# Kernel tuning notes

Measured on AMD Instinct MI355X. Metric: run time of the kernel, lower is better.

The kernel has to match this reference:

```python
import jax, jax.numpy as jnp
import numpy as np

DIM = 512
NUM_EXPERTS = 8
HID = 4 * DIM
B, S = 2, 2048


def setup_inputs() -> dict:
    key = jax.random.key(0)
    ks = jax.random.split(key, 7)
    sc = 0.02
    x = jax.random.normal(ks[0], (B, S, DIM), dtype=jnp.float32)
    Wr = jax.random.normal(ks[1], (DIM, NUM_EXPERTS), dtype=jnp.float32) * sc
    br = jnp.zeros((NUM_EXPERTS,), dtype=jnp.float32)
    W1 = jax.random.normal(ks[2], (NUM_EXPERTS, DIM, HID), dtype=jnp.float32) * sc
    b1 = jnp.zeros((NUM_EXPERTS, HID), dtype=jnp.float32)
    W2 = jax.random.normal(ks[3], (NUM_EXPERTS, HID, DIM), dtype=jnp.float32) * sc
    b2 = jnp.zeros((NUM_EXPERTS, DIM), dtype=jnp.float32)
    return {"x": x, "Wr": Wr, "br": br, "W1": W1, "b1": b1, "W2": W2, "b2": b2}


def reference(x, Wr, br, W1, b1, W2, b2):
    b, s, d = x.shape
    E = Wr.shape[1]
    xf = x.reshape(-1, d)                                   # [N, d]
    N = xf.shape[0]
    logits = xf @ Wr + br                                   # [N, E]
    probs = jax.nn.softmax(logits, axis=-1)
    top_w, top_idx = jax.lax.top_k(probs, 2)                # [N, 2]
    top_w = jax.nn.softmax(top_w, axis=-1)                  # renormalize top-2
    # combine weight per (token, expert); topk indices are distinct so add is safe
    comb = jnp.zeros((N, E), dtype=xf.dtype)
    comb = comb.at[jnp.arange(N)[:, None], top_idx].add(top_w)  # [N, E]
    # dense per-expert MLP (eval mode: dropout is identity); exact GELU as nn.GELU
    h = jax.nn.gelu(jnp.einsum('nd,edf->enf', xf, W1) + b1[:, None, :], approximate=False)
    y = jnp.einsum('enf,efd->end', h, W2) + b2[:, None, :]  # [E, N, d]
    out = jnp.einsum('end,ne->nd', y, comb)                 # weighted combine
    # load-balancing loss
    load = jnp.zeros((E,), dtype=jnp.float32).at[top_idx.reshape(-1)].add(1.0)
    load = load / load.sum()
    lb_loss = jnp.sum((load - 1.0 / E) ** 2)
    return out.reshape(b, s, d), lb_loss, load
```

## Files before the change

kernel.cpp:

```cpp
#include <hip/hip_runtime.h>
#include <hip/hip_bf16.h>

#define DIMD 512
#define NEXP 8
#define HIDN 2048
#define NTOK 4096
#define NASG 8192

typedef short bf16x8 __attribute__((ext_vector_type(8)));
typedef float f32x4 __attribute__((ext_vector_type(4)));

__device__ inline unsigned short f2bf(float f) {
  __hip_bfloat16 h = __float2bfloat16(f);
  return __builtin_bit_cast(unsigned short, h);
}

__device__ inline void gl16(const void* g, void* l) {
  __builtin_amdgcn_global_load_lds(
      (const __attribute__((address_space(1))) unsigned int*)g,
      (__attribute__((address_space(3))) unsigned int*)l, 16, 0, 0);
}

#define PIPE_WAIT4_BAR() do { \
  asm volatile("s_waitcnt vmcnt(4)" ::: "memory"); \
  __builtin_amdgcn_s_barrier(); \
  __builtin_amdgcn_sched_barrier(0); } while (0)
#define PIPE_WAIT0_BAR() do { \
  asm volatile("s_waitcnt vmcnt(0)" ::: "memory"); \
  __builtin_amdgcn_s_barrier(); \
  __builtin_amdgcn_sched_barrier(0); } while (0)
#define PIPE_POST_BAR() do { \
  asm volatile("" ::: "memory"); \
  __builtin_amdgcn_sched_barrier(0); \
  __builtin_amdgcn_s_barrier(); } while (0)

__global__ __launch_bounds__(256) void transpose_both_kernel(
    const float* __restrict__ W1, const float* __restrict__ W2,
    unsigned short* __restrict__ w1t, unsigned short* __restrict__ w2t) {
  __shared__ float tile[64][65];
  int z = blockIdx.z;
  int e = z & 7;
  const float* src; unsigned short* dst; int R, C, r0, c0;
  if (z < 8) { src = W1; dst = w1t; R = DIMD; C = HIDN; c0 = blockIdx.x * 64; r0 = blockIdx.y * 64; }
  else       { src = W2; dst = w2t; R = HIDN; C = DIMD; r0 = blockIdx.x * 64; c0 = blockIdx.y * 64; }
  const float* s = src + (size_t)e * R * C;
  unsigned short* d = dst + (size_t)e * R * C;
  for (int i = threadIdx.x; i < 4096; i += 256) {
    int r = i >> 6, c = i & 63;
    tile[r][c] = s[(size_t)(r0 + r) * C + (c0 + c)];
  }
  __syncthreads();
  for (int i = threadIdx.x; i < 2048; i += 256) {
    int c = i >> 5;
    int r = (i & 31) * 2;
    unsigned lo = f2bf(tile[r][c]);
    unsigned hi = f2bf(tile[r + 1][c]);
    *reinterpret_cast<unsigned*>(d + (size_t)(c0 + c) * R + (r0 + r)) = lo | (hi << 16);
  }
}

__global__ __launch_bounds__(256) void router_kernel(const float* __restrict__ x,
                                                     const float* __restrict__ Wr,
                                                     const float* __restrict__ br,
                                                     int* __restrict__ tidx,
                                                     float* __restrict__ tw,
                                                     unsigned short* __restrict__ xb) {
  int lane = threadIdx.x & 63;
  int n = blockIdx.x * 4 + (threadIdx.x >> 6);
  const float* xr = x + (size_t)n * DIMD;
  unsigned short* xbr = xb + (size_t)n * DIMD;
  float acc[NEXP];
#pragma unroll
  for (int e = 0; e < NEXP; ++e) acc[e] = 0.f;
#pragma unroll
  for (int it = 0; it < 2; ++it) {
    int d0 = it * 256 + lane * 4;
    float4 xv = *reinterpret_cast<const float4*>(xr + d0);
    unsigned p0 = (unsigned)f2bf(xv.x) | ((unsigned)f2bf(xv.y) << 16);
    unsigned p1 = (unsigned)f2bf(xv.z) | ((unsigned)f2bf(xv.w) << 16);
    *reinterpret_cast<uint2*>(xbr + d0) = make_uint2(p0, p1);
    const float* wr = Wr + (size_t)d0 * NEXP;
#pragma unroll
    for (int j = 0; j < 4; ++j) {
      float xj = (&xv.x)[j];
#pragma unroll
      for (int e = 0; e < NEXP; ++e) acc[e] += xj * wr[j * NEXP + e];
    }
  }
#pragma unroll
  for (int e = 0; e < NEXP; ++e) {
    float v = acc[e];
#pragma unroll
    for (int off = 32; off > 0; off >>= 1) v += __shfl_xor(v, off, 64);
    acc[e] = v + br[e];
  }
  if (lane == 0) {
    float m = acc[0];
    for (int e = 1; e < NEXP; ++e) m = fmaxf(m, acc[e]);
    float p[NEXP], s = 0.f;
    for (int e = 0; e < NEXP; ++e) { p[e] = expf(acc[e] - m); s += p[e]; }
    float inv = 1.f / s;
    for (int e = 0; e < NEXP; ++e) p[e] *= inv;
    int i0 = 0; float p0 = p[0];
    for (int e = 1; e < NEXP; ++e) if (p[e] > p0) { p0 = p[e]; i0 = e; }
    int i1 = (i0 == 0) ? 1 : 0; float p1 = p[i1];
    for (int e = 0; e < NEXP; ++e) if (e != i0 && p[e] > p1) { p1 = p[e]; i1 = e; }
    float t = expf(p1 - p0);
    float w0 = 1.f / (1.f + t);
    tidx[2 * n] = i0; tidx[2 * n + 1] = i1;
    tw[2 * n] = w0; tw[2 * n + 1] = t * w0;
  }
}

__global__ __launch_bounds__(1024) void route_pack_kernel(const int* __restrict__ tidx,
                                                          int* __restrict__ off,
                                                          int* __restrict__ list,
                                                          float* __restrict__ out_tail) {
  int tid = threadIdx.x;
  int wv = tid >> 6, lane = tid & 63;

  int ids[8];
#pragma unroll
  for (int j = 0; j < 8; ++j) ids[j] = tidx[tid * 8 + j];

  int c[NEXP];
#pragma unroll
  for (int e = 0; e < NEXP; ++e) c[e] = 0;
#pragma unroll
  for (int j = 0; j < 8; ++j)
#pragma unroll
    for (int e = 0; e < NEXP; ++e) c[e] += (ids[j] == e) ? 1 : 0;

  int inc[NEXP];
#pragma unroll
  for (int e = 0; e < NEXP; ++e) {
    int v = c[e];
#pragma unroll
    for (int d = 1; d < 64; d <<= 1) {
      int t = __shfl_up(v, d, 64);
      if (lane >= d) v += t;
    }
    inc[e] = v;
  }

  __shared__ int wtot[NEXP][16];
  __shared__ int wbase[NEXP][16];
  __shared__ int ebase[NEXP];
  if (lane == 63) {
#pragma unroll
    for (int e = 0; e < NEXP; ++e) wtot[e][wv] = inc[e];
  }
  __syncthreads();
  if (tid == 0) {
    int o = 0;
    float lb = 0.f;
    for (int e = 0; e < NEXP; ++e) {
      int s = 0;
      for (int w = 0; w < 16; ++w) { wbase[e][w] = s; s += wtot[e][w]; }
      ebase[e] = o;
      off[e] = o;
      o += s;
      float l = (float)s / (float)NASG;
      out_tail[1 + e] = l;
      float dd = l - 0.125f;
      lb += dd * dd;
    }
    off[NEXP] = o;
    out_tail[0] = lb;
  }
  __syncthreads();

  int pos[NEXP];
#pragma unroll
  for (int e = 0; e < NEXP; ++e)
    pos[e] = ebase[e] + wbase[e][wv] + (inc[e] - c[e]);

#pragma unroll
  for (int j = 0; j < 8; ++j) {
    int e = ids[j];
    int p = 0;
#pragma unroll
    for (int k = 0; k < NEXP; ++k)
      if (e == k) { p = pos[k]; pos[k] = p + 1; }
    list[p] = tid * 8 + j;
  }
}


__global__ __launch_bounds__(256) void gemm1_kernel(
    const unsigned short* __restrict__ xb,
    const unsigned short* __restrict__ w1t,
    const float* __restrict__ b1,
    const int* __restrict__ off,
    const int* __restrict__ list,
    unsigned short* __restrict__ H) {
  int e = blockIdx.x;
  int offe = off[e];
  int cnt_e = off[e + 1] - offe;
  int n0 = blockIdx.y * 128;
  int m0 = blockIdx.z * 128;
  if (m0 >= cnt_e) return;

  __shared__ char ldsb[36864];

  int tid = threadIdx.x, wv = tid >> 6, lane = tid & 63;
  int rp = lane >> 3, sl = lane & 7;
  int sx = sl ^ rp;
  int rowadd = rp * 2 + (sx >> 2);
  int kq = sx & 3;

  const unsigned short* w1e = w1t + (size_t)e * HIDN * DIMD;
  const unsigned short* asrc[2];
  const unsigned short* bsrc[2];
#pragma unroll
  for (int i = 0; i < 2; ++i) {
    int r = wv * 32 + i * 16 + rowadd;
    int rr = m0 + r;
    int tok = 0;
    if (rr < cnt_e) tok = list[offe + rr] >> 1;
    asrc[i] = xb + (size_t)tok * DIMD + kq * 8;
    bsrc[i] = w1e + (size_t)(n0 + r) * DIMD + kq * 8;
  }
  int dstA0 = wv * 2048;
  int dstA1 = wv * 2048 + 1024;

  f32x4 zero = {0.f, 0.f, 0.f, 0.f};
  f32x4 acc[4][4];
#pragma unroll
  for (int m = 0; m < 4; ++m)
#pragma unroll
    for (int n = 0; n < 4; ++n) acc[m][n] = zero;

  int wave_m = wv >> 1, wave_n = wv & 1;
  int lane16 = lane & 15, kq4 = lane >> 4;
  int ra[4], rb[4];
#pragma unroll
  for (int m = 0; m < 4; ++m) {
    int r = wave_m * 64 + m * 16 + lane16;
    ra[m] = (r >> 1) * 128 + ((((kq4 + (r & 1) * 4)) ^ ((r >> 1) & 7)) << 4);
    int rn = wave_n * 64 + m * 16 + lane16;
    rb[m] = (rn >> 1) * 128 + ((((kq4 + (rn & 1) * 4)) ^ ((rn >> 1) & 7)) << 4);
  }

  auto stage = [&](char* nb, int k0) {
    gl16(asrc[0] + k0, nb + dstA0);
    gl16(asrc[1] + k0, nb + dstA1);
    gl16(bsrc[0] + k0, nb + 8192 + dstA0);
    gl16(bsrc[1] + k0, nb + 8192 + dstA1);
  };
  auto compute = [&](const char* cb) {
    bf16x8 af[4], bfr[4];
#pragma unroll
    for (int m = 0; m < 4; ++m) af[m] = *reinterpret_cast<const bf16x8*>(cb + ra[m]);
#pragma unroll
    for (int n = 0; n < 4; ++n) bfr[n] = *reinterpret_cast<const bf16x8*>(cb + 8192 + rb[n]);
#pragma unroll
    for (int m = 0; m < 4; ++m)
#pragma unroll
      for (int n = 0; n < 4; ++n)
        acc[m][n] = __builtin_amdgcn_mfma_f32_16x16x32_bf16(af[m], bfr[n], acc[m][n], 0, 0, 0);
  };

  const int T = DIMD / 32;
  stage(ldsb, 0);
  stage(ldsb + 16384, 32);
  for (int t = 0; t < T - 2; ++t) {
    char* cb = ldsb + (t & 1) * 16384;
    PIPE_WAIT4_BAR();
    compute(cb);
    PIPE_POST_BAR();
    stage(cb, (t + 2) * 32);
  }
  PIPE_WAIT4_BAR();
  compute(ldsb + ((T - 2) & 1) * 16384);
  PIPE_POST_BAR();
  PIPE_WAIT0_BAR();
  compute(ldsb + ((T - 1) & 1) * 16384);
  PIPE_POST_BAR();

  unsigned short* Ct = (unsigned short*)ldsb;
  const float* b1e = b1 + e * HIDN;
#pragma unroll
  for (int n = 0; n < 4; ++n) {
    int cl = wave_n * 64 + n * 16 + lane16;
    float bias = b1e[n0 + cl];
#pragma unroll
    for (int m = 0; m < 4; ++m) {
#pragma unroll
      for (int q = 0; q < 4; ++q) {
        int rl = wave_m * 64 + m * 16 + kq4 * 4 + q;
        float v = acc[m][n][q] + bias;
        float g = 0.5f * v * (1.f + erff(v * 0.70710678118654752f));
        Ct[rl * 136 + cl] = f2bf(g);
      }
    }
  }
  __syncthreads();
  for (int u = tid; u < 2048; u += 256) {
    int rl = u >> 4, c8 = (u & 15) * 8;
    int r = m0 + rl;
    if (r < cnt_e) {
      uint4 v = *reinterpret_cast<const uint4*>(Ct + rl * 136 + c8);
      *reinterpret_cast<uint4*>(H + (size_t)(offe + r) * HIDN + n0 + c8) = v;
    }
  }
}

__global__ __launch_bounds__(256) void gemm2_kernel(
    const unsigned short* __restrict__ H,
    const unsigned short* __restrict__ w2t,
    const float* __restrict__ b2,
    const int* __restrict__ off,
    const int* __restrict__ list,
    const float* __restrict__ tw,
    float* __restrict__ Yw) {
  int e = blockIdx.x;
  int offe = off[e];
  int cnt_e = off[e + 1] - offe;
  int n0 = blockIdx.y * 128;
  int m0 = blockIdx.z * 128;
  if (m0 >= cnt_e) return;

  __shared__ char ldsb[32768];

  int tid = threadIdx.x, wv = tid >> 6, lane = tid & 63;
  int rp = lane >> 3, sl = lane & 7;
  int sx = sl ^ rp;
  int rowadd = rp * 2 + (sx >> 2);
  int kq = sx & 3;

  const unsigned short* w2e = w2t + (size_t)e * DIMD * HIDN;
  const unsigned short* asrc[2];
  const unsigned short* bsrc[2];
#pragma unroll
  for (int i = 0; i < 2; ++i) {
    int r = wv * 32 + i * 16 + rowadd;
    int rowa = offe + m0 + r;
    if (rowa > NASG - 1) rowa = NASG - 1;
    asrc[i] = H + (size_t)rowa * HIDN + kq * 8;
    bsrc[i] = w2e + (size_t)(n0 + r) * HIDN + kq * 8;
  }
  int dstA0 = wv * 2048;
  int dstA1 = wv * 2048 + 1024;

  f32x4 zero = {0.f, 0.f, 0.f, 0.f};
  f32x4 acc[4][4];
#pragma unroll
  for (int m = 0; m < 4; ++m)
#pragma unroll
    for (int n = 0; n < 4; ++n) acc[m][n] = zero;

  int wave_m = wv >> 1, wave_n = wv & 1;
  int lane16 = lane & 15, kq4 = lane >> 4;
  int ra[4], rb[4];
#pragma unroll
  for (int m = 0; m < 4; ++m) {
    int r = wave_m * 64 + m * 16 + lane16;
    ra[m] = (r >> 1) * 128 + ((((kq4 + (r & 1) * 4)) ^ ((r >> 1) & 7)) << 4);
    int rn = wave_n * 64 + m * 16 + lane16;
    rb[m] = (rn >> 1) * 128 + ((((kq4 + (rn & 1) * 4)) ^ ((rn >> 1) & 7)) << 4);
  }

  auto stage = [&](char* nb, int k0) {
    gl16(asrc[0] + k0, nb + dstA0);
    gl16(asrc[1] + k0, nb + dstA1);
    gl16(bsrc[0] + k0, nb + 8192 + dstA0);
    gl16(bsrc[1] + k0, nb + 8192 + dstA1);
  };
  auto compute = [&](const char* cb) {
    bf16x8 af[4], bfr[4];
#pragma unroll
    for (int m = 0; m < 4; ++m) af[m] = *reinterpret_cast<const bf16x8*>(cb + ra[m]);
#pragma unroll
    for (int n = 0; n < 4; ++n) bfr[n] = *reinterpret_cast<const bf16x8*>(cb + 8192 + rb[n]);
#pragma unroll
    for (int m = 0; m < 4; ++m)
#pragma unroll
      for (int n = 0; n < 4; ++n)
        acc[m][n] = __builtin_amdgcn_mfma_f32_16x16x32_bf16(af[m], bfr[n], acc[m][n], 0, 0, 0);
  };

  const int T = HIDN / 32;
  stage(ldsb, 0);
  stage(ldsb + 16384, 32);
  for (int t = 0; t < T - 2; ++t) {
    char* cb = ldsb + (t & 1) * 16384;
    PIPE_WAIT4_BAR();
    compute(cb);
    PIPE_POST_BAR();
    stage(cb, (t + 2) * 32);
  }
  PIPE_WAIT4_BAR();
  compute(ldsb + ((T - 2) & 1) * 16384);
  PIPE_POST_BAR();
  PIPE_WAIT0_BAR();
  compute(ldsb + ((T - 1) & 1) * 16384);
  PIPE_POST_BAR();

  const float* b2e = b2 + e * DIMD;
  float bias[4];
#pragma unroll
  for (int n = 0; n < 4; ++n) bias[n] = b2e[n0 + wave_n * 64 + n * 16 + lane16];
#pragma unroll
  for (int m = 0; m < 4; ++m) {
#pragma unroll
    for (int q = 0; q < 4; ++q) {
      int r = m0 + wave_m * 64 + m * 16 + kq4 * 4 + q;
      if (r < cnt_e) {
        int a = list[offe + r];
        float w = tw[a];
        float* yrow = Yw + (size_t)a * DIMD;
#pragma unroll
        for (int n = 0; n < 4; ++n) {
          int col = n0 + wave_n * 64 + n * 16 + lane16;
          yrow[col] = w * (acc[m][n][q] + bias[n]);
        }
      }
    }
  }
}

__global__ __launch_bounds__(256) void combine_kernel(const float* __restrict__ Yw,
                                                      float* __restrict__ out) {
  int i = (blockIdx.x * 256 + threadIdx.x) * 4;
  int n = i >> 9;
  int d = i & 511;
  float4 a = *reinterpret_cast<const float4*>(Yw + (size_t)(2 * n) * DIMD + d);
  float4 b = *reinterpret_cast<const float4*>(Yw + (size_t)(2 * n + 1) * DIMD + d);
  float4 o;
  o.x = a.x + b.x; o.y = a.y + b.y; o.z = a.z + b.z; o.w = a.w + b.w;
  *reinterpret_cast<float4*>(out + i) = o;
}

extern "C" void kernel_launch(void* const* d_in, const int* in_sizes, int n_in,
                              void* d_out, int out_size, void* d_ws, size_t ws_size,
                              hipStream_t stream) {
  const float* x  = (const float*)d_in[0];
  const float* Wr = (const float*)d_in[1];
  const float* br = (const float*)d_in[2];
  const float* W1 = (const float*)d_in[3];
  const float* b1 = (const float*)d_in[4];
  const float* W2 = (const float*)d_in[5];
  const float* b2 = (const float*)d_in[6];
  float* out = (float*)d_out;

  char* ws = (char*)d_ws;
  unsigned short* xb  = (unsigned short*)ws;  ws += (size_t)NTOK * DIMD * 2;
  unsigned short* w1t = (unsigned short*)ws;  ws += (size_t)NEXP * HIDN * DIMD * 2;
  unsigned short* w2t = (unsigned short*)ws;  ws += (size_t)NEXP * DIMD * HIDN * 2;
  unsigned short* H   = (unsigned short*)ws;  ws += (size_t)NASG * HIDN * 2;
  float* Yw = (float*)ws;                     ws += (size_t)NASG * DIMD * 4;
  float* tw = (float*)ws;                     ws += (size_t)NASG * 4;
  int* tidx = (int*)ws;                       ws += (size_t)NASG * 4;
  int* list = (int*)ws;                       ws += (size_t)NASG * 4;
  int* offp = (int*)ws;

  transpose_both_kernel<<<dim3(32, 8, 16), 256, 0, stream>>>(W1, W2, w1t, w2t);
  router_kernel<<<NTOK / 4, 256, 0, stream>>>(x, Wr, br, tidx, tw, xb);
  route_pack_kernel<<<1, 1024, 0, stream>>>(tidx, offp, list, out + (size_t)NTOK * DIMD);
  gemm1_kernel<<<dim3(NEXP, HIDN / 128, NASG / 128), 256, 0, stream>>>(xb, w1t, b1, offp, list, H);
  gemm2_kernel<<<dim3(NEXP, DIMD / 128, NASG / 128), 256, 0, stream>>>(H, w2t, b2, offp, list, tw, Yw);
  combine_kernel<<<2048, 256, 0, stream>>>(Yw, out);
}
```

Before: 118.3 us.

## Use 256-row M tiles, triple-buffered pipeline, split-K gemm2 with combine epilogue

```diff
diff --git a/kernel.cpp b/kernel.cpp
--- a/kernel.cpp
+++ b/kernel.cpp
@@ -21,8 +21,12 @@
       (__attribute__((address_space(3))) unsigned int*)l, 16, 0, 0);
 }
 
-#define PIPE_WAIT4_BAR() do { \
-  asm volatile("s_waitcnt vmcnt(4)" ::: "memory"); \
+#define PIPE_WAIT12_BAR() do { \
+  asm volatile("s_waitcnt vmcnt(12)" ::: "memory"); \
+  __builtin_amdgcn_s_barrier(); \
+  __builtin_amdgcn_sched_barrier(0); } while (0)
+#define PIPE_WAIT6_BAR() do { \
+  asm volatile("s_waitcnt vmcnt(6)" ::: "memory"); \
   __builtin_amdgcn_s_barrier(); \
   __builtin_amdgcn_sched_barrier(0); } while (0)
 #define PIPE_WAIT0_BAR() do { \
@@ -187,7 +191,7 @@
 }
 
 
-__global__ __launch_bounds__(256) void gemm1_kernel(
+__global__ __launch_bounds__(256, 2) void gemm1_kernel(
     const unsigned short* __restrict__ xb,
     const unsigned short* __restrict__ w1t,
     const float* __restrict__ b1,
@@ -198,10 +202,10 @@
   int offe = off[e];
   int cnt_e = off[e + 1] - offe;
   int n0 = blockIdx.y * 128;
-  int m0 = blockIdx.z * 128;
+  int m0 = blockIdx.z * 256;
   if (m0 >= cnt_e) return;
 
-  __shared__ char ldsb[36864];
+  __shared__ char ldsb[73728];
 
   int tid = threadIdx.x, wv = tid >> 6, lane = tid & 63;
   int rp = lane >> 3, sl = lane & 7;
@@ -210,52 +214,61 @@
   int kq = sx & 3;
 
   const unsigned short* w1e = w1t + (size_t)e * HIDN * DIMD;
-  const unsigned short* asrc[2];
+  const unsigned short* asrc[4];
   const unsigned short* bsrc[2];
 #pragma unroll
-  for (int i = 0; i < 2; ++i) {
-    int r = wv * 32 + i * 16 + rowadd;
+  for (int i = 0; i < 4; ++i) {
+    int r = wv * 64 + i * 16 + rowadd;
     int rr = m0 + r;
     int tok = 0;
     if (rr < cnt_e) tok = list[offe + rr] >> 1;
     asrc[i] = xb + (size_t)tok * DIMD + kq * 8;
+  }
+#pragma unroll
+  for (int i = 0; i < 2; ++i) {
+    int r = wv * 32 + i * 16 + rowadd;
     bsrc[i] = w1e + (size_t)(n0 + r) * DIMD + kq * 8;
   }
-  int dstA0 = wv * 2048;
-  int dstA1 = wv * 2048 + 1024;
+  int dA = wv * 4096;
+  int dB = 16384 + wv * 2048;
 
   f32x4 zero = {0.f, 0.f, 0.f, 0.f};
-  f32x4 acc[4][4];
-#pragma unroll
-  for (int m = 0; m < 4; ++m)
+  f32x4 acc[8][4];
+#pragma unroll
+  for (int m = 0; m < 8; ++m)
 #pragma unroll
     for (int n = 0; n < 4; ++n) acc[m][n] = zero;
 
   int wave_m = wv >> 1, wave_n = wv & 1;
   int lane16 = lane & 15, kq4 = lane >> 4;
-  int ra[4], rb[4];
-#pragma unroll
-  for (int m = 0; m < 4; ++m) {
-    int r = wave_m * 64 + m * 16 + lane16;
+  int ra[8], rb[4];
+#pragma unroll
+  for (int m = 0; m < 8; ++m) {
+    int r = wave_m * 128 + m * 16 + lane16;
     ra[m] = (r >> 1) * 128 + ((((kq4 + (r & 1) * 4)) ^ ((r >> 1) & 7)) << 4);
-    int rn = wave_n * 64 + m * 16 + lane16;
-    rb[m] = (rn >> 1) * 128 + ((((kq4 + (rn & 1) * 4)) ^ ((rn >> 1) & 7)) << 4);
+  }
+#pragma unroll
+  for (int n = 0; n < 4; ++n) {
+    int rn = wave_n * 64 + n * 16 + lane16;
+    rb[n] = (rn >> 1) * 128 + ((((kq4 + (rn & 1) * 4)) ^ ((rn >> 1) & 7)) << 4);
   }
 
   auto stage = [&](char* nb, int k0) {
-    gl16(asrc[0] + k0, nb + dstA0);
-    gl16(asrc[1] + k0, nb + dstA1);
-    gl16(bsrc[0] + k0, nb + 8192 + dstA0);
-    gl16(bsrc[1] + k0, nb + 8192 + dstA1);
+    gl16(asrc[0] + k0, nb + dA);
+    gl16(asrc[1] + k0, nb + dA + 1024);
+    gl16(asrc[2] + k0, nb + dA + 2048);
+    gl16(asrc[3] + k0, nb + dA + 3072);
+    gl16(bsrc[0] + k0, nb + dB);
+    gl16(bsrc[1] + k0, nb + dB + 1024);
   };
   auto compute = [&](const char* cb) {
-    bf16x8 af[4], bfr[4];
-#pragma unroll
-    for (int m = 0; m < 4; ++m) af[m] = *reinterpret_cast<const bf16x8*>(cb + ra[m]);
-#pragma unroll
-    for (int n = 0; n < 4; ++n) bfr[n] = *reinterpret_cast<const bf16x8*>(cb + 8192 + rb[n]);
-#pragma unroll
-    for (int m = 0; m < 4; ++m)
+    bf16x8 af[8], bfr[4];
+#pragma unroll
+    for (int m = 0; m < 8; ++m) af[m] = *reinterpret_cast<const bf16x8*>(cb + ra[m]);
+#pragma unroll
+    for (int n = 0; n < 4; ++n) bfr[n] = *reinterpret_cast<const bf16x8*>(cb + 16384 + rb[n]);
+#pragma unroll
+    for (int m = 0; m < 8; ++m)
 #pragma unroll
       for (int n = 0; n < 4; ++n)
         acc[m][n] = __builtin_amdgcn_mfma_f32_16x16x32_bf16(af[m], bfr[n], acc[m][n], 0, 0, 0);
@@ -263,65 +276,69 @@
 
   const int T = DIMD / 32;
   stage(ldsb, 0);
-  stage(ldsb + 16384, 32);
-  for (int t = 0; t < T - 2; ++t) {
-    char* cb = ldsb + (t & 1) * 16384;
-    PIPE_WAIT4_BAR();
+  stage(ldsb + 24576, 32);
+  stage(ldsb + 49152, 64);
+  int cyc = 0;
+  for (int t = 0; t < T; ++t) {
+    char* cb = ldsb + cyc * 24576;
+    if (t <= T - 3) PIPE_WAIT12_BAR();
+    else if (t == T - 2) PIPE_WAIT6_BAR();
+    else PIPE_WAIT0_BAR();
     compute(cb);
     PIPE_POST_BAR();
-    stage(cb, (t + 2) * 32);
-  }
-  PIPE_WAIT4_BAR();
-  compute(ldsb + ((T - 2) & 1) * 16384);
-  PIPE_POST_BAR();
-  PIPE_WAIT0_BAR();
-  compute(ldsb + ((T - 1) & 1) * 16384);
-  PIPE_POST_BAR();
+    if (t <= T - 4) stage(cb, (t + 3) * 32);
+    cyc = (cyc == 2) ? 0 : cyc + 1;
+  }
 
   unsigned short* Ct = (unsigned short*)ldsb;
   const float* b1e = b1 + e * HIDN;
-#pragma unroll
-  for (int n = 0; n < 4; ++n) {
-    int cl = wave_n * 64 + n * 16 + lane16;
-    float bias = b1e[n0 + cl];
-#pragma unroll
-    for (int m = 0; m < 4; ++m) {
-#pragma unroll
-      for (int q = 0; q < 4; ++q) {
-        int rl = wave_m * 64 + m * 16 + kq4 * 4 + q;
-        float v = acc[m][n][q] + bias;
-        float g = 0.5f * v * (1.f + erff(v * 0.70710678118654752f));
-        Ct[rl * 136 + cl] = f2bf(g);
+  for (int c = 0; c < 2; ++c) {
+    if (wave_m == c) {
+#pragma unroll
+      for (int n = 0; n < 4; ++n) {
+        int cl = wave_n * 64 + n * 16 + lane16;
+        float bias = b1e[n0 + cl];
+#pragma unroll
+        for (int m = 0; m < 8; ++m) {
+#pragma unroll
+          for (int q = 0; q < 4; ++q) {
+            int rl = m * 16 + kq4 * 4 + q;
+            float v = acc[m][n][q] + bias;
+            float g = 0.5f * v * (1.f + erff(v * 0.70710678118654752f));
+            Ct[rl * 136 + cl] = f2bf(g);
+          }
+        }
       }
     }
-  }
-  __syncthreads();
-  for (int u = tid; u < 2048; u += 256) {
-    int rl = u >> 4, c8 = (u & 15) * 8;
-    int r = m0 + rl;
-    if (r < cnt_e) {
-      uint4 v = *reinterpret_cast<const uint4*>(Ct + rl * 136 + c8);
-      *reinterpret_cast<uint4*>(H + (size_t)(offe + r) * HIDN + n0 + c8) = v;
-    }
-  }
-}
-
-__global__ __launch_bounds__(256) void gemm2_kernel(
+    __syncthreads();
+    for (int u = tid; u < 2048; u += 256) {
+      int rl = u >> 4, c8 = (u & 15) * 8;
+      int r = m0 + c * 128 + rl;
+      if (r < cnt_e) {
+        uint4 v = *reinterpret_cast<const uint4*>(Ct + rl * 136 + c8);
+        *reinterpret_cast<uint4*>(H + (size_t)(offe + r) * HIDN + n0 + c8) = v;
+      }
+    }
+    __syncthreads();
+  }
+}
+
+__global__ __launch_bounds__(256, 2) void gemm2_kernel(
     const unsigned short* __restrict__ H,
     const unsigned short* __restrict__ w2t,
-    const float* __restrict__ b2,
     const int* __restrict__ off,
     const int* __restrict__ list,
-    const float* __restrict__ tw,
     float* __restrict__ Yw) {
   int e = blockIdx.x;
   int offe = off[e];
   int cnt_e = off[e + 1] - offe;
-  int n0 = blockIdx.y * 128;
-  int m0 = blockIdx.z * 128;
+  int n0 = (blockIdx.y >> 1) * 128;
+  int khalf = blockIdx.y & 1;
+  int kbase = khalf * (HIDN / 2);
+  int m0 = blockIdx.z * 256;
   if (m0 >= cnt_e) return;
 
-  __shared__ char ldsb[32768];
+  __shared__ char ldsb[73728];
 
   int tid = threadIdx.x, wv = tid >> 6, lane = tid & 63;
   int rp = lane >> 3, sl = lane & 7;
@@ -330,90 +347,94 @@
   int kq = sx & 3;
 
   const unsigned short* w2e = w2t + (size_t)e * DIMD * HIDN;
-  const unsigned short* asrc[2];
+  const unsigned short* asrc[4];
   const unsigned short* bsrc[2];
+#pragma unroll
+  for (int i = 0; i < 4; ++i) {
+    int r = wv * 64 + i * 16 + rowadd;
+    int rowa = offe + m0 + r;
+    if (rowa > NASG - 1) rowa = NASG - 1;
+    asrc[i] = H + (size_t)rowa * HIDN + kbase + kq * 8;
+  }
 #pragma unroll
   for (int i = 0; i < 2; ++i) {
     int r = wv * 32 + i * 16 + rowadd;
-    int rowa = offe + m0 + r;
-    if (rowa > NASG - 1) rowa = NASG - 1;
-    asrc[i] = H + (size_t)rowa * HIDN + kq * 8;
-    bsrc[i] = w2e + (size_t)(n0 + r) * HIDN + kq * 8;
-  }
-  int dstA0 = wv * 2048;
-  int dstA1 = wv * 2048 + 1024;
+    bsrc[i] = w2e + (size_t)(n0 + r) * HIDN + kbase + kq * 8;
+  }
+  int dA = wv * 4096;
+  int dB = 16384 + wv * 2048;
 
   f32x4 zero = {0.f, 0.f, 0.f, 0.f};
-  f32x4 acc[4][4];
-#pragma unroll
-  for (int m = 0; m < 4; ++m)
+  f32x4 acc[8][4];
+#pragma unroll
+  for (int m = 0; m < 8; ++m)
 #pragma unroll
     for (int n = 0; n < 4; ++n) acc[m][n] = zero;
 
   int wave_m = wv >> 1, wave_n = wv & 1;
   int lane16 = lane & 15, kq4 = lane >> 4;
-  int ra[4], rb[4];
-#pragma unroll
-  for (int m = 0; m < 4; ++m) {
-    int r = wave_m * 64 + m * 16 + lane16;
+  int ra[8], rb[4];
+#pragma unroll
+  for (int m = 0; m < 8; ++m) {
+    int r = wave_m * 128 + m * 16 + lane16;
     ra[m] = (r >> 1) * 128 + ((((kq4 + (r & 1) * 4)) ^ ((r >> 1) & 7)) << 4);
-    int rn = wave_n * 64 + m * 16 + lane16;
-    rb[m] = (rn >> 1) * 128 + ((((kq4 + (rn & 1) * 4)) ^ ((rn >> 1) & 7)) << 4);
+  }
+#pragma unroll
+  for (int n = 0; n < 4; ++n) {
+    int rn = wave_n * 64 + n * 16 + lane16;
+    rb[n] = (rn >> 1) * 128 + ((((kq4 + (rn & 1) * 4)) ^ ((rn >> 1) & 7)) << 4);
   }
 
   auto stage = [&](char* nb, int k0) {
-    gl16(asrc[0] + k0, nb + dstA0);
-    gl16(asrc[1] + k0, nb + dstA1);
-    gl16(bsrc[0] + k0, nb + 8192 + dstA0);
-    gl16(bsrc[1] + k0, nb + 8192 + dstA1);
+    gl16(asrc[0] + k0, nb + dA);
+    gl16(asrc[1] + k0, nb + dA + 1024);
+    gl16(asrc[2] + k0, nb + dA + 2048);
+    gl16(asrc[3] + k0, nb + dA + 3072);
+    gl16(bsrc[0] + k0, nb + dB);
+    gl16(bsrc[1] + k0, nb + dB + 1024);
   };
   auto compute = [&](const char* cb) {
-    bf16x8 af[4], bfr[4];
-#pragma unroll
-    for (int m = 0; m < 4; ++m) af[m] = *reinterpret_cast<const bf16x8*>(cb + ra[m]);
-#pragma unroll
-    for (int n = 0; n < 4; ++n) bfr[n] = *reinterpret_cast<const bf16x8*>(cb + 8192 + rb[n]);
-#pragma unroll
-    for (int m = 0; m < 4; ++m)
+    bf16x8 af[8], bfr[4];
+#pragma unroll
+    for (int m = 0; m < 8; ++m) af[m] = *reinterpret_cast<const bf16x8*>(cb + ra[m]);
+#pragma unroll
+    for (int n = 0; n < 4; ++n) bfr[n] = *reinterpret_cast<const bf16x8*>(cb + 16384 + rb[n]);
+#pragma unroll
+    for (int m = 0; m < 8; ++m)
 #pragma unroll
       for (int n = 0; n < 4; ++n)
         acc[m][n] = __builtin_amdgcn_mfma_f32_16x16x32_bf16(af[m], bfr[n], acc[m][n], 0, 0, 0);
   };
 
-  const int T = HIDN / 32;
+  const int T = (HIDN / 2) / 32;
   stage(ldsb, 0);
-  stage(ldsb + 16384, 32);
-  for (int t = 0; t < T - 2; ++t) {
-    char* cb = ldsb + (t & 1) * 16384;
-    PIPE_WAIT4_BAR();
+  stage(ldsb + 24576, 32);
+  stage(ldsb + 49152, 64);
+  int cyc = 0;
+  for (int t = 0; t < T; ++t) {
+    char* cb = ldsb + cyc * 24576;
+    if (t <= T - 3) PIPE_WAIT12_BAR();
+    else if (t == T - 2) PIPE_WAIT6_BAR();
+    else PIPE_WAIT0_BAR();
     compute(cb);
     PIPE_POST_BAR();
-    stage(cb, (t + 2) * 32);
-  }
-  PIPE_WAIT4_BAR();
-  compute(ldsb + ((T - 2) & 1) * 16384);
-  PIPE_POST_BAR();
-  PIPE_WAIT0_BAR();
-  compute(ldsb + ((T - 1) & 1) * 16384);
-  PIPE_POST_BAR();
-
-  const float* b2e = b2 + e * DIMD;
-  float bias[4];
-#pragma unroll
-  for (int n = 0; n < 4; ++n) bias[n] = b2e[n0 + wave_n * 64 + n * 16 + lane16];
-#pragma unroll
-  for (int m = 0; m < 4; ++m) {
+    if (t <= T - 4) stage(cb, (t + 3) * 32);
+    cyc = (cyc == 2) ? 0 : cyc + 1;
+  }
+
+  float* Ywp = Yw + (size_t)khalf * NASG * DIMD;
+#pragma unroll
+  for (int m = 0; m < 8; ++m) {
 #pragma unroll
     for (int q = 0; q < 4; ++q) {
-      int r = m0 + wave_m * 64 + m * 16 + kq4 * 4 + q;
+      int r = m0 + wave_m * 128 + m * 16 + kq4 * 4 + q;
       if (r < cnt_e) {
         int a = list[offe + r];
-        float w = tw[a];
-        float* yrow = Yw + (size_t)a * DIMD;
+        float* yrow = Ywp + (size_t)a * DIMD;
 #pragma unroll
         for (int n = 0; n < 4; ++n) {
           int col = n0 + wave_n * 64 + n * 16 + lane16;
-          yrow[col] = w * (acc[m][n][q] + bias[n]);
+          yrow[col] = acc[m][n][q];
         }
       }
     }
@@ -421,14 +442,28 @@
 }
 
 __global__ __launch_bounds__(256) void combine_kernel(const float* __restrict__ Yw,
+                                                      const int* __restrict__ tidx,
+                                                      const float* __restrict__ tw,
+                                                      const float* __restrict__ b2,
                                                       float* __restrict__ out) {
+  const float* Y1 = Yw + (size_t)NASG * DIMD;
   int i = (blockIdx.x * 256 + threadIdx.x) * 4;
   int n = i >> 9;
   int d = i & 511;
-  float4 a = *reinterpret_cast<const float4*>(Yw + (size_t)(2 * n) * DIMD + d);
-  float4 b = *reinterpret_cast<const float4*>(Yw + (size_t)(2 * n + 1) * DIMD + d);
+  int a0 = 2 * n, a1 = 2 * n + 1;
+  float w0 = tw[a0], w1 = tw[a1];
+  int e0 = tidx[a0], e1 = tidx[a1];
+  float4 p0 = *reinterpret_cast<const float4*>(Yw + (size_t)a0 * DIMD + d);
+  float4 q0 = *reinterpret_cast<const float4*>(Y1 + (size_t)a0 * DIMD + d);
+  float4 p1 = *reinterpret_cast<const float4*>(Yw + (size_t)a1 * DIMD + d);
+  float4 q1 = *reinterpret_cast<const float4*>(Y1 + (size_t)a1 * DIMD + d);
+  float4 c0 = *reinterpret_cast<const float4*>(b2 + (size_t)e0 * DIMD + d);
+  float4 c1 = *reinterpret_cast<const float4*>(b2 + (size_t)e1 * DIMD + d);
   float4 o;
-  o.x = a.x + b.x; o.y = a.y + b.y; o.z = a.z + b.z; o.w = a.w + b.w;
+  o.x = w0 * (p0.x + q0.x + c0.x) + w1 * (p1.x + q1.x + c1.x);
+  o.y = w0 * (p0.y + q0.y + c0.y) + w1 * (p1.y + q1.y + c1.y);
+  o.z = w0 * (p0.z + q0.z + c0.z) + w1 * (p1.z + q1.z + c1.z);
+  o.w = w0 * (p0.w + q0.w + c0.w) + w1 * (p1.w + q1.w + c1.w);
   *reinterpret_cast<float4*>(out + i) = o;
 }
 
@@ -449,7 +484,7 @@
   unsigned short* w1t = (unsigned short*)ws;  ws += (size_t)NEXP * HIDN * DIMD * 2;
   unsigned short* w2t = (unsigned short*)ws;  ws += (size_t)NEXP * DIMD * HIDN * 2;
   unsigned short* H   = (unsigned short*)ws;  ws += (size_t)NASG * HIDN * 2;
-  float* Yw = (float*)ws;                     ws += (size_t)NASG * DIMD * 4;
+  float* Yw = (float*)ws;                     ws += (size_t)2 * NASG * DIMD * 4;
   float* tw = (float*)ws;                     ws += (size_t)NASG * 4;
   int* tidx = (int*)ws;                       ws += (size_t)NASG * 4;
   int* list = (int*)ws;                       ws += (size_t)NASG * 4;
@@ -458,7 +493,7 @@
   transpose_both_kernel<<<dim3(32, 8, 16), 256, 0, stream>>>(W1, W2, w1t, w2t);
   router_kernel<<<NTOK / 4, 256, 0, stream>>>(x, Wr, br, tidx, tw, xb);
   route_pack_kernel<<<1, 1024, 0, stream>>>(tidx, offp, list, out + (size_t)NTOK * DIMD);
-  gemm1_kernel<<<dim3(NEXP, HIDN / 128, NASG / 128), 256, 0, stream>>>(xb, w1t, b1, offp, list, H);
-  gemm2_kernel<<<dim3(NEXP, DIMD / 128, NASG / 128), 256, 0, stream>>>(H, w2t, b2, offp, list, tw, Yw);
-  combine_kernel<<<2048, 256, 0, stream>>>(Yw, out);
-}
+  gemm1_kernel<<<dim3(NEXP, HIDN / 128, NASG / 256), 256, 0, stream>>>(xb, w1t, b1, offp, list, H);
+  gemm2_kernel<<<dim3(NEXP, (DIMD / 128) * 2, NASG / 256), 256, 0, stream>>>(H, w2t, offp, list, Yw);
+  combine_kernel<<<2048, 256, 0, stream>>>(Yw, tidx, tw, b2, out);
+}
```

Result: slower. 145.5 us (+23.0%).

## Split gemm2 along K into two halves with 64-wide N tiles, reduce in combine

Applied to the files above, without the earlier changes.

```diff
diff --git a/kernel.cpp b/kernel.cpp
--- a/kernel.cpp
+++ b/kernel.cpp
@@ -23,6 +23,10 @@
 
 #define PIPE_WAIT4_BAR() do { \
   asm volatile("s_waitcnt vmcnt(4)" ::: "memory"); \
+  __builtin_amdgcn_s_barrier(); \
+  __builtin_amdgcn_sched_barrier(0); } while (0)
+#define PIPE_WAIT3_BAR() do { \
+  asm volatile("s_waitcnt vmcnt(3)" ::: "memory"); \
   __builtin_amdgcn_s_barrier(); \
   __builtin_amdgcn_sched_barrier(0); } while (0)
 #define PIPE_WAIT0_BAR() do { \
@@ -309,19 +313,20 @@
 __global__ __launch_bounds__(256) void gemm2_kernel(
     const unsigned short* __restrict__ H,
     const unsigned short* __restrict__ w2t,
-    const float* __restrict__ b2,
     const int* __restrict__ off,
     const int* __restrict__ list,
-    const float* __restrict__ tw,
     float* __restrict__ Yw) {
   int e = blockIdx.x;
   int offe = off[e];
   int cnt_e = off[e + 1] - offe;
-  int n0 = blockIdx.y * 128;
+  int y = blockIdx.y;
+  int khalf = y >> 3;
+  int n0 = (y & 7) * 64;
+  int kbase = khalf * (HIDN / 2);
   int m0 = blockIdx.z * 128;
   if (m0 >= cnt_e) return;
 
-  __shared__ char ldsb[32768];
+  __shared__ char ldsb[24576];
 
   int tid = threadIdx.x, wv = tid >> 6, lane = tid & 63;
   int rp = lane >> 3, sl = lane & 7;
@@ -331,76 +336,74 @@
 
   const unsigned short* w2e = w2t + (size_t)e * DIMD * HIDN;
   const unsigned short* asrc[2];
-  const unsigned short* bsrc[2];
+  const unsigned short* bsrc0;
 #pragma unroll
   for (int i = 0; i < 2; ++i) {
     int r = wv * 32 + i * 16 + rowadd;
     int rowa = offe + m0 + r;
     if (rowa > NASG - 1) rowa = NASG - 1;
-    asrc[i] = H + (size_t)rowa * HIDN + kq * 8;
-    bsrc[i] = w2e + (size_t)(n0 + r) * HIDN + kq * 8;
-  }
-  int dstA0 = wv * 2048;
-  int dstA1 = wv * 2048 + 1024;
+    asrc[i] = H + (size_t)rowa * HIDN + kbase + kq * 8;
+  }
+  {
+    int r = wv * 16 + rowadd;
+    bsrc0 = w2e + (size_t)(n0 + r) * HIDN + kbase + kq * 8;
+  }
+  int dA0 = wv * 2048;
+  int dA1 = wv * 2048 + 1024;
+  int dB = 8192 + wv * 1024;
 
   f32x4 zero = {0.f, 0.f, 0.f, 0.f};
-  f32x4 acc[4][4];
+  f32x4 acc[4][2];
 #pragma unroll
   for (int m = 0; m < 4; ++m)
 #pragma unroll
-    for (int n = 0; n < 4; ++n) acc[m][n] = zero;
+    for (int n = 0; n < 2; ++n) acc[m][n] = zero;
 
   int wave_m = wv >> 1, wave_n = wv & 1;
   int lane16 = lane & 15, kq4 = lane >> 4;
-  int ra[4], rb[4];
+  int ra[4], rb[2];
 #pragma unroll
   for (int m = 0; m < 4; ++m) {
     int r = wave_m * 64 + m * 16 + lane16;
     ra[m] = (r >> 1) * 128 + ((((kq4 + (r & 1) * 4)) ^ ((r >> 1) & 7)) << 4);
-    int rn = wave_n * 64 + m * 16 + lane16;
-    rb[m] = (rn >> 1) * 128 + ((((kq4 + (rn & 1) * 4)) ^ ((rn >> 1) & 7)) << 4);
+  }
+#pragma unroll
+  for (int n = 0; n < 2; ++n) {
+    int rn = wave_n * 32 + n * 16 + lane16;
+    rb[n] = (rn >> 1) * 128 + ((((kq4 + (rn & 1) * 4)) ^ ((rn >> 1) & 7)) << 4);
   }
 
   auto stage = [&](char* nb, int k0) {
-    gl16(asrc[0] + k0, nb + dstA0);
-    gl16(asrc[1] + k0, nb + dstA1);
-    gl16(bsrc[0] + k0, nb + 8192 + dstA0);
-    gl16(bsrc[1] + k0, nb + 8192 + dstA1);
+    gl16(asrc[0] + k0, nb + dA0);
+    gl16(asrc[1] + k0, nb + dA1);
+    gl16(bsrc0 + k0, nb + dB);
   };
   auto compute = [&](const char* cb) {
-    bf16x8 af[4], bfr[4];
+    bf16x8 af[4], bfr[2];
 #pragma unroll
     for (int m = 0; m < 4; ++m) af[m] = *reinterpret_cast<const bf16x8*>(cb + ra[m]);
 #pragma unroll
-    for (int n = 0; n < 4; ++n) bfr[n] = *reinterpret_cast<const bf16x8*>(cb + 8192 + rb[n]);
+    for (int n = 0; n < 2; ++n) bfr[n] = *reinterpret_cast<const bf16x8*>(cb + 8192 + rb[n]);
 #pragma unroll
     for (int m = 0; m < 4; ++m)
 #pragma unroll
-      for (int n = 0; n < 4; ++n)
+      for (int n = 0; n < 2; ++n)
         acc[m][n] = __builtin_amdgcn_mfma_f32_16x16x32_bf16(af[m], bfr[n], acc[m][n], 0, 0, 0);
   };
 
-  const int T = HIDN / 32;
+  const int T = (HIDN / 2) / 32;
   stage(ldsb, 0);
-  stage(ldsb + 16384, 32);
-  for (int t = 0; t < T - 2; ++t) {
-    char* cb = ldsb + (t & 1) * 16384;
-    PIPE_WAIT4_BAR();
+  stage(ldsb + 12288, 32);
+  for (int t = 0; t < T; ++t) {
+    char* cb = ldsb + (t & 1) * 12288;
+    if (t < T - 1) PIPE_WAIT3_BAR();
+    else PIPE_WAIT0_BAR();
     compute(cb);
     PIPE_POST_BAR();
-    stage(cb, (t + 2) * 32);
-  }
-  PIPE_WAIT4_BAR();
-  compute(ldsb + ((T - 2) & 1) * 16384);
-  PIPE_POST_BAR();
-  PIPE_WAIT0_BAR();
-  compute(ldsb + ((T - 1) & 1) * 16384);
-  PIPE_POST_BAR();
-
-  const float* b2e = b2 + e * DIMD;
-  float bias[4];
-#pragma unroll
-  for (int n = 0; n < 4; ++n) bias[n] = b2e[n0 + wave_n * 64 + n * 16 + lane16];
+    if (t < T - 2) stage(cb, (t + 2) * 32);
+  }
+
+  float* Ywp = Yw + (size_t)khalf * NASG * DIMD;
 #pragma unroll
   for (int m = 0; m < 4; ++m) {
 #pragma unroll
@@ -408,12 +411,11 @@
       int r = m0 + wave_m * 64 + m * 16 + kq4 * 4 + q;
       if (r < cnt_e) {
         int a = list[offe + r];
-        float w = tw[a];
-        float* yrow = Yw + (size_t)a * DIMD;
-#pragma unroll
-        for (int n = 0; n < 4; ++n) {
-          int col = n0 + wave_n * 64 + n * 16 + lane16;
-          yrow[col] = w * (acc[m][n][q] + bias[n]);
+        float* yrow = Ywp + (size_t)a * DIMD;
+#pragma unroll
+        for (int n = 0; n < 2; ++n) {
+          int col = n0 + wave_n * 32 + n * 16 + lane16;
+          yrow[col] = acc[m][n][q];
         }
       }
     }
@@ -421,14 +423,28 @@
 }
 
 __global__ __launch_bounds__(256) void combine_kernel(const float* __restrict__ Yw,
+                                                      const int* __restrict__ tidx,
+                                                      const float* __restrict__ tw,
+                                                      const float* __restrict__ b2,
                                                       float* __restrict__ out) {
+  const float* Y1 = Yw + (size_t)NASG * DIMD;
   int i = (blockIdx.x * 256 + threadIdx.x) * 4;
   int n = i >> 9;
   int d = i & 511;
-  float4 a = *reinterpret_cast<const float4*>(Yw + (size_t)(2 * n) * DIMD + d);
-  float4 b = *reinterpret_cast<const float4*>(Yw + (size_t)(2 * n + 1) * DIMD + d);
+  int a0 = 2 * n, a1 = 2 * n + 1;
+  float w0 = tw[a0], w1 = tw[a1];
+  int e0 = tidx[a0], e1 = tidx[a1];
+  float4 p0 = *reinterpret_cast<const float4*>(Yw + (size_t)a0 * DIMD + d);
+  float4 q0 = *reinterpret_cast<const float4*>(Y1 + (size_t)a0 * DIMD + d);
+  float4 p1 = *reinterpret_cast<const float4*>(Yw + (size_t)a1 * DIMD + d);
+  float4 q1 = *reinterpret_cast<const float4*>(Y1 + (size_t)a1 * DIMD + d);
+  float4 c0 = *reinterpret_cast<const float4*>(b2 + (size_t)e0 * DIMD + d);
+  float4 c1 = *reinterpret_cast<const float4*>(b2 + (size_t)e1 * DIMD + d);
   float4 o;
-  o.x = a.x + b.x; o.y = a.y + b.y; o.z = a.z + b.z; o.w = a.w + b.w;
+  o.x = w0 * (p0.x + q0.x + c0.x) + w1 * (p1.x + q1.x + c1.x);
+  o.y = w0 * (p0.y + q0.y + c0.y) + w1 * (p1.y + q1.y + c1.y);
+  o.z = w0 * (p0.z + q0.z + c0.z) + w1 * (p1.z + q1.z + c1.z);
+  o.w = w0 * (p0.w + q0.w + c0.w) + w1 * (p1.w + q1.w + c1.w);
   *reinterpret_cast<float4*>(out + i) = o;
 }
 
@@ -449,7 +465,7 @@
   unsigned short* w1t = (unsigned short*)ws;  ws += (size_t)NEXP * HIDN * DIMD * 2;
   unsigned short* w2t = (unsigned short*)ws;  ws += (size_t)NEXP * DIMD * HIDN * 2;
   unsigned short* H   = (unsigned short*)ws;  ws += (size_t)NASG * HIDN * 2;
-  float* Yw = (float*)ws;                     ws += (size_t)NASG * DIMD * 4;
+  float* Yw = (float*)ws;                     ws += (size_t)2 * NASG * DIMD * 4;
   float* tw = (float*)ws;                     ws += (size_t)NASG * 4;
   int* tidx = (int*)ws;                       ws += (size_t)NASG * 4;
   int* list = (int*)ws;                       ws += (size_t)NASG * 4;
@@ -459,6 +475,6 @@
   router_kernel<<<NTOK / 4, 256, 0, stream>>>(x, Wr, br, tidx, tw, xb);
   route_pack_kernel<<<1, 1024, 0, stream>>>(tidx, offp, list, out + (size_t)NTOK * DIMD);
   gemm1_kernel<<<dim3(NEXP, HIDN / 128, NASG / 128), 256, 0, stream>>>(xb, w1t, b1, offp, list, H);
-  gemm2_kernel<<<dim3(NEXP, DIMD / 128, NASG / 128), 256, 0, stream>>>(H, w2t, b2, offp, list, tw, Yw);
-  combine_kernel<<<2048, 256, 0, stream>>>(Yw, out);
-}
+  gemm2_kernel<<<dim3(NEXP, 16, NASG / 128), 256, 0, stream>>>(H, w2t, offp, list, Yw);
+  combine_kernel<<<2048, 256, 0, stream>>>(Yw, tidx, tw, b2, out);
+}
```

After: 120.5 us. No clear change (+1.9%).

## Restructure gemm1 into 256x256 tiles with 512 threads and phased MFMA pipeline

Applied to the files above, without the earlier changes.

```diff
diff --git a/kernel.cpp b/kernel.cpp
--- a/kernel.cpp
+++ b/kernel.cpp
@@ -21,6 +21,10 @@
       (__attribute__((address_space(3))) unsigned int*)l, 16, 0, 0);
 }
 
+#define PIPE_WAIT8_BAR() do { \
+  asm volatile("s_waitcnt vmcnt(8)" ::: "memory"); \
+  __builtin_amdgcn_s_barrier(); \
+  __builtin_amdgcn_sched_barrier(0); } while (0)
 #define PIPE_WAIT4_BAR() do { \
   asm volatile("s_waitcnt vmcnt(4)" ::: "memory"); \
   __builtin_amdgcn_s_barrier(); \
@@ -33,6 +37,9 @@
   asm volatile("" ::: "memory"); \
   __builtin_amdgcn_sched_barrier(0); \
   __builtin_amdgcn_s_barrier(); } while (0)
+#define PIPE_MID_BAR() do { \
+  __builtin_amdgcn_s_barrier(); \
+  __builtin_amdgcn_sched_barrier(0); } while (0)
 
 __global__ __launch_bounds__(256) void transpose_both_kernel(
     const float* __restrict__ W1, const float* __restrict__ W2,
@@ -187,7 +194,28 @@
 }
 
 
-__global__ __launch_bounds__(256) void gemm1_kernel(
+#define G1_PHASE(F0) do { \
+  const char* Ah_ = A + ((F0) >> 2) * 16384; \
+  int r0_ = (wave_m * 64 + (((F0)) & 3) * 16 + lane16) * 128; \
+  int r1_ = (wave_m * 64 + (((F0) + 1) & 3) * 16 + lane16) * 128; \
+  bf16x8 a00 = *reinterpret_cast<const bf16x8*>(Ah_ + r0_ + sw0); \
+  bf16x8 a01 = *reinterpret_cast<const bf16x8*>(Ah_ + r0_ + sw1); \
+  bf16x8 a10 = *reinterpret_cast<const bf16x8*>(Ah_ + r1_ + sw0); \
+  bf16x8 a11 = *reinterpret_cast<const bf16x8*>(Ah_ + r1_ + sw1); \
+  PIPE_MID_BAR(); \
+  __builtin_amdgcn_s_setprio(1); \
+  _Pragma("unroll") \
+  for (int n_ = 0; n_ < 4; ++n_) { \
+    acc[(F0)][n_]     = __builtin_amdgcn_mfma_f32_16x16x32_bf16(a00, breg[n_][0], acc[(F0)][n_], 0, 0, 0); \
+    acc[(F0)][n_]     = __builtin_amdgcn_mfma_f32_16x16x32_bf16(a01, breg[n_][1], acc[(F0)][n_], 0, 0, 0); \
+    acc[(F0) + 1][n_] = __builtin_amdgcn_mfma_f32_16x16x32_bf16(a10, breg[n_][0], acc[(F0) + 1][n_], 0, 0, 0); \
+    acc[(F0) + 1][n_] = __builtin_amdgcn_mfma_f32_16x16x32_bf16(a11, breg[n_][1], acc[(F0) + 1][n_], 0, 0, 0); \
+  } \
+  __builtin_amdgcn_s_setprio(0); \
+  PIPE_POST_BAR(); \
+} while (0)
+
+__global__ __launch_bounds__(512, 2) void gemm1_kernel(
     const unsigned short* __restrict__ xb,
     const unsigned short* __restrict__ w1t,
     const float* __restrict__ b1,
@@ -197,112 +225,119 @@
   int e = blockIdx.x;
   int offe = off[e];
   int cnt_e = off[e + 1] - offe;
-  int n0 = blockIdx.y * 128;
-  int m0 = blockIdx.z * 128;
+  int n0 = blockIdx.y * 256;
+  int m0 = blockIdx.z * 256;
   if (m0 >= cnt_e) return;
 
-  __shared__ char ldsb[36864];
+  __shared__ char ldsb[131072];
 
   int tid = threadIdx.x, wv = tid >> 6, lane = tid & 63;
-  int rp = lane >> 3, sl = lane & 7;
-  int sx = sl ^ rp;
-  int rowadd = rp * 2 + (sx >> 2);
-  int kq = sx & 3;
+  int wave_m = wv >> 2, wave_n = wv & 3;
+  int lane16 = lane & 15, kq4 = lane >> 4;
+  int ks = (lane & 7) ^ ((lane >> 3) & 7);
+  int rl = lane >> 3;
 
   const unsigned short* w1e = w1t + (size_t)e * HIDN * DIMD;
-  const unsigned short* asrc[2];
-  const unsigned short* bsrc[2];
-#pragma unroll
-  for (int i = 0; i < 2; ++i) {
-    int r = wv * 32 + i * 16 + rowadd;
-    int rr = m0 + r;
-    int tok = 0;
-    if (rr < cnt_e) tok = list[offe + rr] >> 1;
-    asrc[i] = xb + (size_t)tok * DIMD + kq * 8;
-    bsrc[i] = w1e + (size_t)(n0 + r) * DIMD + kq * 8;
-  }
-  int dstA0 = wv * 2048;
-  int dstA1 = wv * 2048 + 1024;
+
+  const unsigned short* aptr[2][2];
+  const unsigned short* bptr[2][2];
+#pragma unroll
+  for (int h = 0; h < 2; ++h) {
+#pragma unroll
+    for (int i = 0; i < 2; ++i) {
+      int r = (wv * 2 + i) * 8 + rl;
+      int grow = m0 + h * 128 + r;
+      int tok = 0;
+      if (grow < cnt_e) tok = list[offe + grow] >> 1;
+      aptr[h][i] = xb + (size_t)tok * DIMD + ks * 8;
+      bptr[h][i] = w1e + (size_t)(n0 + h * 128 + r) * DIMD + ks * 8;
+    }
+  }
+
+  auto stA = [&](int kt2, int h) {
+    char* base = ldsb + (kt2 & 1) * 32768 + h * 16384 + wv * 2048;
+    gl16(aptr[h][0] + kt2 * 64, base);
+    gl16(aptr[h][1] + kt2 * 64, base + 1024);
+  };
+  auto stB = [&](int kt2) {
+    char* base = ldsb + 65536 + (kt2 & 1) * 32768 + wv * 2048;
+    gl16(bptr[0][0] + kt2 * 64, base);
+    gl16(bptr[0][1] + kt2 * 64, base + 1024);
+    gl16(bptr[1][0] + kt2 * 64, base + 16384);
+    gl16(bptr[1][1] + kt2 * 64, base + 16384 + 1024);
+  };
+
+  int sw0 = ((0 + kq4) ^ (lane16 & 7)) << 4;
+  int sw1 = ((4 + kq4) ^ (lane16 & 7)) << 4;
 
   f32x4 zero = {0.f, 0.f, 0.f, 0.f};
-  f32x4 acc[4][4];
-#pragma unroll
-  for (int m = 0; m < 4; ++m)
+  f32x4 acc[8][4];
+#pragma unroll
+  for (int m = 0; m < 8; ++m)
 #pragma unroll
     for (int n = 0; n < 4; ++n) acc[m][n] = zero;
 
-  int wave_m = wv >> 1, wave_n = wv & 1;
-  int lane16 = lane & 15, kq4 = lane >> 4;
-  int ra[4], rb[4];
-#pragma unroll
-  for (int m = 0; m < 4; ++m) {
-    int r = wave_m * 64 + m * 16 + lane16;
-    ra[m] = (r >> 1) * 128 + ((((kq4 + (r & 1) * 4)) ^ ((r >> 1) & 7)) << 4);
-    int rn = wave_n * 64 + m * 16 + lane16;
-    rb[m] = (rn >> 1) * 128 + ((((kq4 + (rn & 1) * 4)) ^ ((rn >> 1) & 7)) << 4);
-  }
-
-  auto stage = [&](char* nb, int k0) {
-    gl16(asrc[0] + k0, nb + dstA0);
-    gl16(asrc[1] + k0, nb + dstA1);
-    gl16(bsrc[0] + k0, nb + 8192 + dstA0);
-    gl16(bsrc[1] + k0, nb + 8192 + dstA1);
-  };
-  auto compute = [&](const char* cb) {
-    bf16x8 af[4], bfr[4];
-#pragma unroll
-    for (int m = 0; m < 4; ++m) af[m] = *reinterpret_cast<const bf16x8*>(cb + ra[m]);
-#pragma unroll
-    for (int n = 0; n < 4; ++n) bfr[n] = *reinterpret_cast<const bf16x8*>(cb + 8192 + rb[n]);
-#pragma unroll
-    for (int m = 0; m < 4; ++m)
-#pragma unroll
-      for (int n = 0; n < 4; ++n)
-        acc[m][n] = __builtin_amdgcn_mfma_f32_16x16x32_bf16(af[m], bfr[n], acc[m][n], 0, 0, 0);
-  };
-
-  const int T = DIMD / 32;
-  stage(ldsb, 0);
-  stage(ldsb + 16384, 32);
-  for (int t = 0; t < T - 2; ++t) {
-    char* cb = ldsb + (t & 1) * 16384;
-    PIPE_WAIT4_BAR();
-    compute(cb);
-    PIPE_POST_BAR();
-    stage(cb, (t + 2) * 32);
-  }
-  PIPE_WAIT4_BAR();
-  compute(ldsb + ((T - 2) & 1) * 16384);
-  PIPE_POST_BAR();
-  PIPE_WAIT0_BAR();
-  compute(ldsb + ((T - 1) & 1) * 16384);
-  PIPE_POST_BAR();
+  stB(0); stA(0, 0); stA(0, 1);
+  stB(1); stA(1, 0); stA(1, 1);
+
+  const int NT = DIMD / 64;
+  for (int kt = 0; kt < NT; ++kt) {
+    const char* A = ldsb + (kt & 1) * 32768;
+    const char* B = ldsb + 65536 + (kt & 1) * 32768;
+    if (kt < NT - 1) PIPE_WAIT8_BAR(); else PIPE_WAIT0_BAR();
+
+    bf16x8 breg[4][2];
+    {
+      const char* Bh = B + (wave_n >> 1) * 16384;
+      int rb = ((wave_n & 1) * 64 + lane16) * 128;
+#pragma unroll
+      for (int n = 0; n < 4; ++n) {
+        breg[n][0] = *reinterpret_cast<const bf16x8*>(Bh + rb + n * 2048 + sw0);
+        breg[n][1] = *reinterpret_cast<const bf16x8*>(Bh + rb + n * 2048 + sw1);
+      }
+    }
+    G1_PHASE(0);
+    if (kt < NT - 2) stB(kt + 2);
+    G1_PHASE(2);
+    if (kt < NT - 2) stA(kt + 2, 0);
+    G1_PHASE(4);
+    G1_PHASE(6);
+    if (kt < NT - 2) stA(kt + 2, 1);
+  }
 
   unsigned short* Ct = (unsigned short*)ldsb;
   const float* b1e = b1 + e * HIDN;
-#pragma unroll
-  for (int n = 0; n < 4; ++n) {
-    int cl = wave_n * 64 + n * 16 + lane16;
-    float bias = b1e[n0 + cl];
-#pragma unroll
-    for (int m = 0; m < 4; ++m) {
-#pragma unroll
-      for (int q = 0; q < 4; ++q) {
-        int rl = wave_m * 64 + m * 16 + kq4 * 4 + q;
-        float v = acc[m][n][q] + bias;
-        float g = 0.5f * v * (1.f + erff(v * 0.70710678118654752f));
-        Ct[rl * 136 + cl] = f2bf(g);
+  float bias[4];
+#pragma unroll
+  for (int n = 0; n < 4; ++n) bias[n] = b1e[n0 + wave_n * 64 + n * 16 + lane16];
+#pragma unroll
+  for (int h = 0; h < 2; ++h) {
+#pragma unroll
+    for (int fq = 0; fq < 4; ++fq) {
+#pragma unroll
+      for (int n = 0; n < 4; ++n) {
+        int cl = wave_n * 64 + n * 16 + lane16;
+#pragma unroll
+        for (int q = 0; q < 4; ++q) {
+          int rl2 = wave_m * 64 + fq * 16 + kq4 * 4 + q;
+          float v = acc[h * 4 + fq][n][q] + bias[n];
+          float g = 0.5f * v * (1.f + erff(v * 0.70710678118654752f));
+          Ct[rl2 * 264 + cl] = f2bf(g);
+        }
       }
     }
-  }
-  __syncthreads();
-  for (int u = tid; u < 2048; u += 256) {
-    int rl = u >> 4, c8 = (u & 15) * 8;
-    int r = m0 + rl;
-    if (r < cnt_e) {
-      uint4 v = *reinterpret_cast<const uint4*>(Ct + rl * 136 + c8);
-      *reinterpret_cast<uint4*>(H + (size_t)(offe + r) * HIDN + n0 + c8) = v;
-    }
+    __syncthreads();
+#pragma unroll
+    for (int j = 0; j < 8; ++j) {
+      int u = tid + j * 512;
+      int row = u >> 5, c8 = (u & 31) * 8;
+      int grow = m0 + h * 128 + row;
+      if (grow < cnt_e) {
+        uint4 v = *reinterpret_cast<const uint4*>(Ct + row * 264 + c8);
+        *reinterpret_cast<uint4*>(H + (size_t)(offe + grow) * HIDN + n0 + c8) = v;
+      }
+    }
+    __syncthreads();
   }
 }
 
@@ -458,7 +493,7 @@
   transpose_both_kernel<<<dim3(32, 8, 16), 256, 0, stream>>>(W1, W2, w1t, w2t);
   router_kernel<<<NTOK / 4, 256, 0, stream>>>(x, Wr, br, tidx, tw, xb);
   route_pack_kernel<<<1, 1024, 0, stream>>>(tidx, offp, list, out + (size_t)NTOK * DIMD);
-  gemm1_kernel<<<dim3(NEXP, HIDN / 128, NASG / 128), 256, 0, stream>>>(xb, w1t, b1, offp, list, H);
+  gemm1_kernel<<<dim3(NEXP, HIDN / 256, NASG / 256), 512, 0, stream>>>(xb, w1t, b1, offp, list, H);
   gemm2_kernel<<<dim3(NEXP, DIMD / 128, NASG / 128), 256, 0, stream>>>(H, w2t, b2, offp, list, tw, Yw);
   combine_kernel<<<2048, 256, 0, stream>>>(Yw, out);
 }
```

New measurement: 136.1 us. 1.15x slower.
